# Kernel tuning notes

Measured on AMD Instinct MI355X. Metric: run time of the kernel, lower is better.

Reference implementation:

```python
import jax, jax.numpy as jnp
import numpy as np

C_IN = 512
C_QK = C_IN // 8
B, H, W = 8, 96, 96


def setup_inputs() -> dict:
    key = jax.random.key(0)
    ks = jax.random.split(key, 8)
    s = 1.0 / np.sqrt(C_IN)
    return {
        "x": jax.random.normal(ks[0], (B, C_IN, H, W), dtype=jnp.float32),
        "Wq": jax.random.normal(ks[1], (C_QK, C_IN), dtype=jnp.float32) * s,
        "bq": jnp.zeros((C_QK,), dtype=jnp.float32),
        "Wk": jax.random.normal(ks[2], (C_QK, C_IN), dtype=jnp.float32) * s,
        "bk": jnp.zeros((C_QK,), dtype=jnp.float32),
        "Wv": jax.random.normal(ks[3], (C_IN, C_IN), dtype=jnp.float32) * s,
        "bv": jnp.zeros((C_IN,), dtype=jnp.float32),
        "gamma": jnp.zeros((1,), dtype=jnp.float32),
    }


def reference(x, Wq, bq, Wk, bk, Wv, bv, gamma):
    Bb, Cc, Hh, Ww = x.shape
    # 1x1 convs as channel GEMMs
    q = jnp.einsum('bchw,oc->bohw', x, Wq) + bq[None, :, None, None]
    k = jnp.einsum('bchw,oc->bohw', x, Wk) + bk[None, :, None, None]
    v = jnp.einsum('bchw,oc->bohw', x, Wv) + bv[None, :, None, None]
    # vertical (column) energy: query at (h,w) vs keys at (g,w); diag h==g masked to -inf
    eH = jnp.einsum('bchw,bcgw->bhwg', q, k)  # [B,H,W,H]
    diag = jnp.eye(Hh, dtype=bool)[:, None, :]  # [H,1,H] broadcasts over w
    eH = jnp.where(diag[None], -jnp.inf, eH)
    # horizontal (row) energy: query at (h,w) vs keys at (h,u)
    eW = jnp.einsum('bchw,bchu->bhwu', q, k)  # [B,H,W,W]
    # joint softmax over concatenated H+W axis
    att = jax.nn.softmax(jnp.concatenate([eH, eW], axis=-1), axis=-1)
    aH, aW = att[..., :Hh], att[..., Hh:]
    out_H = jnp.einsum('bhwg,bcgw->bchw', aH, v)
    out_W = jnp.einsum('bhwu,bchu->bchw', aW, v)
    return gamma * (out_H + out_W) + x
```

## Files before the change

### kernel.cpp

```cpp
#include <hip/hip_runtime.h>
#include <math.h>

constexpr int nB = 8;
constexpr int nC = 512;
constexpr int nH = 96;
constexpr int nW = 96;
constexpr int nP = nH * nW;
constexpr int nCQK = 64;
constexpr int nS = nH + nW;
constexpr int nO = 640;
constexpr int nM = nB * nP;

using short8  = __attribute__((ext_vector_type(8))) short;
using ushort8 = __attribute__((ext_vector_type(8))) unsigned short;
using floatx4 = __attribute__((ext_vector_type(4))) float;

__device__ inline unsigned pack_bf16(float a, float b) {
    unsigned ua = __float_as_uint(a), ub = __float_as_uint(b);
    ua = (ua + 0x7fff + ((ua >> 16) & 1)) >> 16;
    ub = (ub + 0x7fff + ((ub >> 16) & 1)) >> 16;
    return ua | (ub << 16);
}
__device__ inline ushort f2bf(float a) {
    unsigned ua = __float_as_uint(a);
    return (ushort)((ua + 0x7fff + ((ua >> 16) & 1)) >> 16);
}
__device__ inline float bf2f(ushort u) {
    return __uint_as_float((unsigned)u << 16);
}

typedef __attribute__((address_space(3))) unsigned int lds_u32;
typedef __attribute__((address_space(1))) const unsigned int glb_u32;
__device__ inline void gl_lds16(const void* g, void* l) {
    __builtin_amdgcn_global_load_lds((glb_u32*)g, (lds_u32*)l, 16, 0, 0);
}

__global__ __launch_bounds__(256) void transpose_kernel(
    const float* __restrict__ x, ushort* __restrict__ xT)
{
    __shared__ float T[64 * 65];
    const int b = blockIdx.z, p0 = blockIdx.x * 64, c0 = blockIdx.y * 64;
    const int tid = threadIdx.x;
    #pragma unroll
    for (int it = 0; it < 4; ++it) {
        int c  = it * 16 + (tid >> 4);
        int p4 = (tid & 15) * 4;
        float4 v = *(const float4*)&x[((size_t)b * nC + c0 + c) * nP + p0 + p4];
        T[c * 65 + p4 + 0] = v.x; T[c * 65 + p4 + 1] = v.y;
        T[c * 65 + p4 + 2] = v.z; T[c * 65 + p4 + 3] = v.w;
    }
    __syncthreads();
    #pragma unroll
    for (int it = 0; it < 8; ++it) {
        int idx = it * 256 + tid;
        int p = idx >> 5;
        int c = (idx & 31) * 2;
        unsigned u = pack_bf16(T[c * 65 + p], T[(c + 1) * 65 + p]);
        *(unsigned*)&xT[((size_t)b * nP + p0 + p) * nC + c0 + c] = u;
    }
}

__global__ __launch_bounds__(256) void wconv_kernel(
    const float* __restrict__ Wq, const float* __restrict__ bq,
    const float* __restrict__ Wk, const float* __restrict__ bk,
    const float* __restrict__ Wv, const float* __restrict__ bv,
    ushort* __restrict__ Wc, float* __restrict__ bc)
{
    const int o = blockIdx.x, t = threadIdx.x;
    const float *src, *bsrc; int oo;
    if (o < 64)       { src = Wq; bsrc = bq; oo = o; }
    else if (o < 128) { src = Wk; bsrc = bk; oo = o - 64; }
    else              { src = Wv; bsrc = bv; oo = o - 128; }
    float2 v = *(const float2*)&src[(size_t)oo * nC + t * 2];
    *(unsigned*)&Wc[(size_t)o * nC + t * 2] = pack_bf16(v.x, v.y);
    if (t == 0) bc[o] = bsrc[oo];
}

__global__ __launch_bounds__(256) void mfma_proj_kernel(
    const ushort* __restrict__ xT, const ushort* __restrict__ Wc,
    const float* __restrict__ bc, float* __restrict__ qk,
    ushort* __restrict__ vW)
{
    __shared__ ushort As[3][128 * 32];
    __shared__ ushort Bs[3][128 * 32];
    const int tid = threadIdx.x;

    constexpr int NWG   = (nM / 128) * (nO / 128);
    constexpr int CHUNK = NWG / 8;
    const int bid = blockIdx.x;
    const int wg  = (bid & 7) * CHUNK + (bid >> 3);
    const int mtile = wg / 5, ntile = wg % 5;
    const int m0 = mtile * 128, o0 = ntile * 128;

    const int lane = tid & 63;
    const int wave = tid >> 6;

    const int srow = wave * 16 + (lane >> 2);
    const int schk = ((lane & 3) ^ ((lane >> 3) & 3)) * 8;
    const ushort* gA0 = xT + (size_t)(m0 + srow) * nC + schk;
    const ushort* gA1 = gA0 + (size_t)64 * nC;
    const ushort* gB0 = Wc + (size_t)(o0 + srow) * nC + schk;
    const ushort* gB1 = gB0 + (size_t)64 * nC;
    const int lbase  = wave * 16 * 32;
    const int lbase1 = lbase + 64 * 32;

    const int wr = wave & 1, wcl = wave >> 1;
    const int lm = lane & 15, q = lane >> 4;
    const int rsw = (lm >> 1) & 3;
    int aoff[4], boff[4];
    #pragma unroll
    for (int i = 0; i < 4; ++i)
        aoff[i] = (wr * 64 + i * 16 + lm) * 32 + ((q ^ rsw) * 8);
    #pragma unroll
    for (int j = 0; j < 4; ++j)
        boff[j] = (wcl * 64 + j * 16 + lm) * 32 + ((q ^ rsw) * 8);

    floatx4 acc[4][4];
    #pragma unroll
    for (int i = 0; i < 4; ++i)
        #pragma unroll
        for (int j = 0; j < 4; ++j) acc[i][j] = (floatx4){0.f, 0.f, 0.f, 0.f};

    const bool vmode = (ntile != 0);

    gl_lds16(gA0, &As[0][lbase]); gl_lds16(gA1, &As[0][lbase1]);
    gl_lds16(gB0, &Bs[0][lbase]); gl_lds16(gB1, &Bs[0][lbase1]);
    gl_lds16(gA0 + 32, &As[1][lbase]); gl_lds16(gA1 + 32, &As[1][lbase1]);
    gl_lds16(gB0 + 32, &Bs[1][lbase]); gl_lds16(gB1 + 32, &Bs[1][lbase1]);

    #pragma unroll
    for (int t = 0; t < 16; ++t) {
        if (t < 15) asm volatile("s_waitcnt vmcnt(4)" ::: "memory");
        else        asm volatile("s_waitcnt vmcnt(0)" ::: "memory");
        __builtin_amdgcn_s_barrier();
        __builtin_amdgcn_sched_barrier(0);
        if (t < 14) {
            const int nb = (t + 2) % 3;
            const int k0 = (t + 2) * 32;
            gl_lds16(gA0 + k0, &As[nb][lbase]);
            gl_lds16(gA1 + k0, &As[nb][lbase1]);
            gl_lds16(gB0 + k0, &Bs[nb][lbase]);
            gl_lds16(gB1 + k0, &Bs[nb][lbase1]);
        }
        const int cur = t % 3;
        short8 av[4], bvv[4];
        #pragma unroll
        for (int i = 0; i < 4; ++i) av[i] = *(const short8*)&As[cur][aoff[i]];
        #pragma unroll
        for (int j = 0; j < 4; ++j) bvv[j] = *(const short8*)&Bs[cur][boff[j]];
        if (!vmode) {
            #pragma unroll
            for (int i = 0; i < 4; ++i)
                #pragma unroll
                for (int j = 0; j < 4; ++j)
                    acc[i][j] = __builtin_amdgcn_mfma_f32_16x16x32_bf16(
                        av[i], bvv[j], acc[i][j], 0, 0, 0);
        } else {
            #pragma unroll
            for (int i = 0; i < 4; ++i)
                #pragma unroll
                for (int j = 0; j < 4; ++j)
                    acc[i][j] = __builtin_amdgcn_mfma_f32_16x16x32_bf16(
                        bvv[i], av[j], acc[i][j], 0, 0, 0);
        }
    }

    if (!vmode) {
        float bj[4];
        #pragma unroll
        for (int j = 0; j < 4; ++j) bj[j] = bc[wcl * 64 + j * 16 + lm];
        #pragma unroll
        for (int i = 0; i < 4; ++i) {
            #pragma unroll
            for (int r = 0; r < 4; ++r) {
                int mrow = m0 + wr * 64 + i * 16 + q * 4 + r;
                float* orow = qk + (size_t)mrow * 128 + wcl * 64 + lm;
                #pragma unroll
                for (int j = 0; j < 4; ++j) orow[j * 16] = acc[i][j][r] + bj[j];
            }
        }
    } else {
        const int b  = m0 / nP;
        const int p0 = m0 - b * nP;
        #pragma unroll
        for (int i = 0; i < 4; ++i) {
            #pragma unroll
            for (int r = 0; r < 4; ++r) {
                int o = o0 + wcl * 64 + i * 16 + q * 4 + r;
                float bias = bc[o];
                int c = o - 128;
                ushort* vrow = vW + ((size_t)(b * nC + c)) * nP + p0 + wr * 64 + lm;
                #pragma unroll
                for (int j = 0; j < 4; ++j)
                    vrow[j * 16] = f2bf(acc[i][j][r] + bias);
            }
        }
    }
}

__global__ __launch_bounds__(256) void vtrans_kernel(
    const ushort* __restrict__ vW, ushort* __restrict__ vH)
{
    __shared__ ushort T[96 * 128];
    const int c = blockIdx.x, b = blockIdx.y, tid = threadIdx.x;
    const size_t base = ((size_t)(b * nC + c)) * nP;
    for (int l = tid; l < 96 * 12; l += 256) {
        int hh = l / 12, seg = l % 12;
        uint4 u = *(const uint4*)&vW[base + (size_t)hh * nW + seg * 8];
        *(uint4*)&T[hh * 128 + ((seg ^ ((hh >> 3) & 7)) * 8)] = u;
    }
    __syncthreads();
    for (int l = tid; l < 96 * 12; l += 256) {
        int ww = l / 12, seg = l % 12;
        ushort8 vv;
        #pragma unroll
        for (int e = 0; e < 8; ++e) {
            int hh = seg * 8 + e;
            int phys = (((ww >> 3) ^ ((hh >> 3) & 7)) * 8) + (ww & 7);
            vv[e] = T[hh * 128 + phys];
        }
        *(ushort8*)&vH[base + (size_t)ww * nH + seg * 8] = vv;
    }
}

__global__ __launch_bounds__(256) void score_kernel(
    const float* __restrict__ qk, float* __restrict__ att, int mode)
{
    __shared__ float Qs[96][68];
    __shared__ float Ks[96][68];
    const int b   = blockIdx.y;
    const int fix = blockIdx.x;
    const int tid = threadIdx.x;

    for (int l = tid; l < 96 * 16; l += 256) {
        int r  = l / 16;
        int c4 = (l % 16) * 4;
        size_t p = (mode == 0) ? ((size_t)r * nW + fix) : ((size_t)fix * nW + r);
        const float* row = &qk[((size_t)b * nP + p) * 128];
        *(float4*)&Qs[r][c4] = *(const float4*)&row[c4];
        *(float4*)&Ks[r][c4] = *(const float4*)&row[64 + c4];
    }
    __syncthreads();

    const int tx = tid % 16;
    const int ty = tid / 16;
    float acc[6][6] = {};
    for (int c4 = 0; c4 < nCQK; c4 += 4) {
        float4 qv[6], kv[6];
        #pragma unroll
        for (int i = 0; i < 6; ++i) qv[i] = *(const float4*)&Qs[ty + 16 * i][c4];
        #pragma unroll
        for (int j = 0; j < 6; ++j) kv[j] = *(const float4*)&Ks[tx + 16 * j][c4];
        #pragma unroll
        for (int i = 0; i < 6; ++i)
            #pragma unroll
            for (int j = 0; j < 6; ++j)
                acc[i][j] += qv[i].x * kv[j].x + qv[i].y * kv[j].y
                           + qv[i].z * kv[j].z + qv[i].w * kv[j].w;
    }

    #pragma unroll
    for (int i = 0; i < 6; ++i) {
        int row = ty + 16 * i;
        #pragma unroll
        for (int j = 0; j < 6; ++j) {
            int col = tx + 16 * j;
            float val = acc[i][j];
            if (mode == 0) {
                if (col == row) val = -INFINITY;
                att[((size_t)b * nP + row * nW + fix) * nS + col] = val;
            } else {
                att[((size_t)b * nP + fix * nW + row) * nS + 96 + col] = val;
            }
        }
    }
}

__global__ __launch_bounds__(256) void softmax_kernel(
    const float* __restrict__ att, ushort* __restrict__ attb)
{
    const int wav  = threadIdx.x / 64;
    const int lane = threadIdx.x % 64;
    const size_t pix = (size_t)blockIdx.x * 4 + wav;
    const float* a = att + pix * nS;
    ushort* ab = attb + pix * nS;
    float v0 = a[lane], v1 = a[lane + 64], v2 = a[lane + 128];
    float m = fmaxf(fmaxf(v0, v1), v2);
    #pragma unroll
    for (int off = 32; off; off >>= 1) m = fmaxf(m, __shfl_xor(m, off));
    float e0 = __expf(v0 - m), e1 = __expf(v1 - m), e2 = __expf(v2 - m);
    float s = e0 + e1 + e2;
    #pragma unroll
    for (int off = 32; off; off >>= 1) s += __shfl_xor(s, off);
    float inv = 1.0f / s;
    ab[lane]       = f2bf(e0 * inv);
    ab[lane + 64]  = f2bf(e1 * inv);
    ab[lane + 128] = f2bf(e2 * inv);
}

__global__ __launch_bounds__(256) void aggH_kernel(
    const ushort* __restrict__ attb, const ushort* __restrict__ vH,
    ushort* __restrict__ oh)
{
    __shared__ ushort As[96 * 104];
    __shared__ ushort Bs[128 * 104];
    const int b = blockIdx.y, w = blockIdx.x, tid = threadIdx.x;

    for (int l = tid; l < 96 * 12; l += 256) {
        int h = l / 12, seg = l % 12;
        uint4 u = *(const uint4*)&attb[((size_t)(b * nP + h * nW + w)) * nS + seg * 8];
        *(uint4*)&As[h * 104 + seg * 8] = u;
    }
    const int lane = tid & 63, wave = tid >> 6;
    const int wr = wave & 1, wc = wave >> 1;
    const int lm = lane & 15, q = lane >> 4;
    int aoff[3], boff[4];
    #pragma unroll
    for (int i = 0; i < 3; ++i) aoff[i] = (wr * 48 + i * 16 + lm) * 104 + q * 8;
    #pragma unroll
    for (int j = 0; j < 4; ++j) boff[j] = (wc * 64 + j * 16 + lm) * 104 + q * 8;

    for (int ct = 0; ct < 4; ++ct) {
        if (ct) __syncthreads();
        for (int l = tid; l < 128 * 12; l += 256) {
            int cl = l / 12, seg = l % 12;
            uint4 u = *(const uint4*)&vH[((size_t)(b * nC + ct * 128 + cl)) * nP
                                         + w * nH + seg * 8];
            *(uint4*)&Bs[cl * 104 + seg * 8] = u;
        }
        __syncthreads();
        floatx4 acc[3][4];
        #pragma unroll
        for (int i = 0; i < 3; ++i)
            #pragma unroll
            for (int j = 0; j < 4; ++j) acc[i][j] = (floatx4){0.f, 0.f, 0.f, 0.f};
        #pragma unroll
        for (int ks = 0; ks < 3; ++ks) {
            short8 av[3], bvv[4];
            #pragma unroll
            for (int i = 0; i < 3; ++i) av[i] = *(const short8*)&As[aoff[i] + ks * 32];
            #pragma unroll
            for (int j = 0; j < 4; ++j) bvv[j] = *(const short8*)&Bs[boff[j] + ks * 32];
            #pragma unroll
            for (int i = 0; i < 3; ++i)
                #pragma unroll
                for (int j = 0; j < 4; ++j)
                    acc[i][j] = __builtin_amdgcn_mfma_f32_16x16x32_bf16(
                        av[i], bvv[j], acc[i][j], 0, 0, 0);
        }
        #pragma unroll
        for (int i = 0; i < 3; ++i) {
            #pragma unroll
            for (int r = 0; r < 4; ++r) {
                int h = wr * 48 + i * 16 + q * 4 + r;
                ushort* orow = oh + ((size_t)(b * nP + h * nW + w)) * nC
                               + ct * 128 + wc * 64 + lm;
                #pragma unroll
                for (int j = 0; j < 4; ++j) orow[j * 16] = f2bf(acc[i][j][r]);
            }
        }
    }
}

__global__ __launch_bounds__(256) void aggW_kernel(
    const ushort* __restrict__ attb, const ushort* __restrict__ vW,
    const ushort* __restrict__ oh, const float* __restrict__ x,
    const float* __restrict__ gamma, float* __restrict__ out)
{
    __shared__ ushort As[96 * 104];
    __shared__ ushort Bs[64 * 104];
    __shared__ ushort Os[96 * 72];
    const int b = blockIdx.y, h = blockIdx.x, tid = threadIdx.x;
    const float gm = gamma[0];

    for (int l = tid; l < 96 * 12; l += 256) {
        int ww = l / 12, seg = l % 12;
        uint4 u = *(const uint4*)&attb[((size_t)(b * nP + h * nW + ww)) * nS
                                       + 96 + seg * 8];
        *(uint4*)&As[ww * 104 + seg * 8] = u;
    }
    const int lane = tid & 63, wave = tid >> 6;
    const int wr = wave & 1, wc = wave >> 1;
    const int lm = lane & 15, q = lane >> 4;
    int coff[2], woff[3];
    #pragma unroll
    for (int i = 0; i < 2; ++i) coff[i] = (wc * 32 + i * 16 + lm) * 104 + q * 8;
    #pragma unroll
    for (int j = 0; j < 3; ++j) woff[j] = (wr * 48 + j * 16 + lm) * 104 + q * 8;

    for (int ct = 0; ct < 8; ++ct) {
        if (ct) __syncthreads();
        for (int l = tid; l < 64 * 12; l += 256) {
            int cl = l / 12, seg = l % 12;
            uint4 u = *(const uint4*)&vW[((size_t)(b * nC + ct * 64 + cl)) * nP
                                         + h * nW + seg * 8];
            *(uint4*)&Bs[cl * 104 + seg * 8] = u;
        }
        for (int l = tid; l < 96 * 8; l += 256) {
            int ww = l / 8, seg = l % 8;
            uint4 u = *(const uint4*)&oh[((size_t)(b * nP + h * nW + ww)) * nC
                                         + ct * 64 + seg * 8];
            *(uint4*)&Os[ww * 72 + seg * 8] = u;
        }
        __syncthreads();
        floatx4 acc[2][3];
        #pragma unroll
        for (int i = 0; i < 2; ++i)
            #pragma unroll
            for (int j = 0; j < 3; ++j) acc[i][j] = (floatx4){0.f, 0.f, 0.f, 0.f};
        #pragma unroll
        for (int ks = 0; ks < 3; ++ks) {
            short8 cv[2], wv[3];
            #pragma unroll
            for (int i = 0; i < 2; ++i) cv[i] = *(const short8*)&Bs[coff[i] + ks * 32];
            #pragma unroll
            for (int j = 0; j < 3; ++j) wv[j] = *(const short8*)&As[woff[j] + ks * 32];
            #pragma unroll
            for (int i = 0; i < 2; ++i)
                #pragma unroll
                for (int j = 0; j < 3; ++j)
                    acc[i][j] = __builtin_amdgcn_mfma_f32_16x16x32_bf16(
                        cv[i], wv[j], acc[i][j], 0, 0, 0);
        }
        #pragma unroll
        for (int i = 0; i < 2; ++i) {
            #pragma unroll
            for (int r = 0; r < 4; ++r) {
                int cl = wc * 32 + i * 16 + q * 4 + r;
                int c  = ct * 64 + cl;
                #pragma unroll
                for (int j = 0; j < 3; ++j) {
                    int ww = wr * 48 + j * 16 + lm;
                    size_t oidx = ((size_t)(b * nC + c) * nH + h) * nW + ww;
                    float ohv = bf2f(Os[ww * 72 + cl]);
                    out[oidx] = gm * (acc[i][j][r] + ohv) + x[oidx];
                }
            }
        }
    }
}

extern "C" void kernel_launch(void* const* d_in, const int* in_sizes, int n_in,
                              void* d_out, int out_size, void* d_ws, size_t ws_size,
                              hipStream_t stream)
{
    const float* x     = (const float*)d_in[0];
    const float* Wq    = (const float*)d_in[1];
    const float* bq    = (const float*)d_in[2];
    const float* Wk    = (const float*)d_in[3];
    const float* bk    = (const float*)d_in[4];
    const float* Wv    = (const float*)d_in[5];
    const float* bv    = (const float*)d_in[6];
    const float* gamma = (const float*)d_in[7];
    float* out = (float*)d_out;

    char* p = (char*)d_ws;
    ushort* xT  = (ushort*)p;
    ushort* vH  = (ushort*)p;
    p += (size_t)nM * nC * 2;
    float* qk   = (float*)p;
    p += (size_t)nM * 128 * 4;
    ushort* vW  = (ushort*)p;
    p += (size_t)nM * nC * 2;
    float* att  = (float*)p;
    ushort* Wc  = (ushort*)p;
    float* bc   = (float*)(p + (size_t)nO * nC * 2);
    p += (size_t)nM * nS * 4;
    ushort* attb = (ushort*)p;
    p += (size_t)nM * nS * 2;
    ushort* oh  = (ushort*)p;

    dim3 blk(256);
    transpose_kernel<<<dim3(nP / 64, nC / 64, nB), blk, 0, stream>>>(x, xT);
    wconv_kernel<<<dim3(nO), blk, 0, stream>>>(Wq, bq, Wk, bk, Wv, bv, Wc, bc);
    mfma_proj_kernel<<<dim3((nM / 128) * (nO / 128)), blk, 0, stream>>>(xT, Wc, bc, qk, vW);
    vtrans_kernel<<<dim3(nC, nB), blk, 0, stream>>>(vW, vH);
    score_kernel<<<dim3(nW, nB), blk, 0, stream>>>(qk, att, 0);
    score_kernel<<<dim3(nH, nB), blk, 0, stream>>>(qk, att, 1);
    softmax_kernel<<<dim3(nB * nP / 4), blk, 0, stream>>>(att, attb);
    aggH_kernel<<<dim3(nW, nB), blk, 0, stream>>>(attb, vH, oh);
    aggW_kernel<<<dim3(nH, nB), blk, 0, stream>>>(attb, vW, oh, x, gamma, out);
}
```

Baseline: 573.7 us.

## Vectorize stores via LDS staging and deepen projection GEMM pipeline to four buffers

The transpose kernel now writes 16-byte bf16 vectors instead of 4-byte pairs. The projection GEMM moves from a 3-stage to a 4-stage LDS prefetch ring with adjusted vmcnt waits. aggH and aggW stage their MFMA outputs through LDS so global stores (and the x reads in aggW) become coalesced 16-byte accesses instead of scattered 2- or 4-byte writes. This costs extra barriers and LDS reuse; aggW's float staging aliases its Bs/Os buffers.

```diff
diff --git a/kernel.cpp b/kernel.cpp
--- a/kernel.cpp
+++ b/kernel.cpp
@@ -51,12 +51,14 @@
     }
     __syncthreads();
     #pragma unroll
-    for (int it = 0; it < 8; ++it) {
+    for (int it = 0; it < 2; ++it) {
         int idx = it * 256 + tid;
-        int p = idx >> 5;
-        int c = (idx & 31) * 2;
-        unsigned u = pack_bf16(T[c * 65 + p], T[(c + 1) * 65 + p]);
-        *(unsigned*)&xT[((size_t)b * nP + p0 + p) * nC + c0 + c] = u;
+        int p  = idx >> 3;
+        int cc = (idx & 7) * 8;
+        ushort8 v;
+        #pragma unroll
+        for (int e = 0; e < 8; ++e) v[e] = f2bf(T[(cc + e) * 65 + p]);
+        *(ushort8*)&xT[((size_t)b * nP + p0 + p) * nC + c0 + cc] = v;
     }
 }
 
@@ -81,8 +83,8 @@
     const float* __restrict__ bc, float* __restrict__ qk,
     ushort* __restrict__ vW)
 {
-    __shared__ ushort As[3][128 * 32];
-    __shared__ ushort Bs[3][128 * 32];
+    __shared__ ushort As[4][128 * 32];
+    __shared__ ushort Bs[4][128 * 32];
     const int tid = threadIdx.x;
 
     constexpr int NWG   = (nM / 128) * (nO / 128);
@@ -123,26 +125,30 @@
 
     const bool vmode = (ntile != 0);
 
-    gl_lds16(gA0, &As[0][lbase]); gl_lds16(gA1, &As[0][lbase1]);
-    gl_lds16(gB0, &Bs[0][lbase]); gl_lds16(gB1, &Bs[0][lbase1]);
-    gl_lds16(gA0 + 32, &As[1][lbase]); gl_lds16(gA1 + 32, &As[1][lbase1]);
-    gl_lds16(gB0 + 32, &Bs[1][lbase]); gl_lds16(gB1 + 32, &Bs[1][lbase1]);
+    #pragma unroll
+    for (int tt = 0; tt < 3; ++tt) {
+        gl_lds16(gA0 + tt * 32, &As[tt][lbase]);
+        gl_lds16(gA1 + tt * 32, &As[tt][lbase1]);
+        gl_lds16(gB0 + tt * 32, &Bs[tt][lbase]);
+        gl_lds16(gB1 + tt * 32, &Bs[tt][lbase1]);
+    }
 
     #pragma unroll
     for (int t = 0; t < 16; ++t) {
-        if (t < 15) asm volatile("s_waitcnt vmcnt(4)" ::: "memory");
-        else        asm volatile("s_waitcnt vmcnt(0)" ::: "memory");
+        if (t <= 13)      asm volatile("s_waitcnt vmcnt(8)" ::: "memory");
+        else if (t == 14) asm volatile("s_waitcnt vmcnt(4)" ::: "memory");
+        else              asm volatile("s_waitcnt vmcnt(0)" ::: "memory");
         __builtin_amdgcn_s_barrier();
         __builtin_amdgcn_sched_barrier(0);
-        if (t < 14) {
-            const int nb = (t + 2) % 3;
-            const int k0 = (t + 2) * 32;
+        if (t < 13) {
+            const int nb = (t + 3) & 3;
+            const int k0 = (t + 3) * 32;
             gl_lds16(gA0 + k0, &As[nb][lbase]);
             gl_lds16(gA1 + k0, &As[nb][lbase1]);
             gl_lds16(gB0 + k0, &Bs[nb][lbase]);
             gl_lds16(gB1 + k0, &Bs[nb][lbase1]);
         }
-        const int cur = t % 3;
+        const int cur = t & 3;
         short8 av[4], bvv[4];
         #pragma unroll
         for (int i = 0; i < 4; ++i) av[i] = *(const short8*)&As[cur][aoff[i]];
@@ -304,6 +310,7 @@
 {
     __shared__ ushort As[96 * 104];
     __shared__ ushort Bs[128 * 104];
+    ushort* Ot = Bs;
     const int b = blockIdx.y, w = blockIdx.x, tid = threadIdx.x;
 
     for (int l = tid; l < 96 * 12; l += 256) {
@@ -348,16 +355,22 @@
                     acc[i][j] = __builtin_amdgcn_mfma_f32_16x16x32_bf16(
                         av[i], bvv[j], acc[i][j], 0, 0, 0);
         }
+        __syncthreads();
         #pragma unroll
         for (int i = 0; i < 3; ++i) {
             #pragma unroll
             for (int r = 0; r < 4; ++r) {
                 int h = wr * 48 + i * 16 + q * 4 + r;
-                ushort* orow = oh + ((size_t)(b * nP + h * nW + w)) * nC
-                               + ct * 128 + wc * 64 + lm;
-                #pragma unroll
-                for (int j = 0; j < 4; ++j) orow[j * 16] = f2bf(acc[i][j][r]);
+                #pragma unroll
+                for (int j = 0; j < 4; ++j)
+                    Ot[h * 136 + wc * 64 + j * 16 + lm] = f2bf(acc[i][j][r]);
             }
+        }
+        __syncthreads();
+        for (int l = tid; l < 96 * 16; l += 256) {
+            int h = l >> 4, seg = l & 15;
+            *(ushort8*)&oh[((size_t)(b * nP + h * nW + w)) * nC + ct * 128 + seg * 8] =
+                *(const ushort8*)&Ot[h * 136 + seg * 8];
         }
     }
 }
@@ -368,8 +381,10 @@
     const float* __restrict__ gamma, float* __restrict__ out)
 {
     __shared__ ushort As[96 * 104];
-    __shared__ ushort Bs[64 * 104];
-    __shared__ ushort Os[96 * 72];
+    __shared__ ushort BO[64 * 104 + 96 * 72];
+    ushort* Bs = BO;
+    ushort* Os = BO + 64 * 104;
+    float*  Ot = (float*)BO;
     const int b = blockIdx.y, h = blockIdx.x, tid = threadIdx.x;
     const float gm = gamma[0];
 
@@ -422,20 +437,37 @@
                     acc[i][j] = __builtin_amdgcn_mfma_f32_16x16x32_bf16(
                         cv[i], wv[j], acc[i][j], 0, 0, 0);
         }
-        #pragma unroll
-        for (int i = 0; i < 2; ++i) {
+        float sv[2][3][4];
+        #pragma unroll
+        for (int i = 0; i < 2; ++i)
             #pragma unroll
             for (int r = 0; r < 4; ++r) {
                 int cl = wc * 32 + i * 16 + q * 4 + r;
-                int c  = ct * 64 + cl;
                 #pragma unroll
                 for (int j = 0; j < 3; ++j) {
                     int ww = wr * 48 + j * 16 + lm;
-                    size_t oidx = ((size_t)(b * nC + c) * nH + h) * nW + ww;
-                    float ohv = bf2f(Os[ww * 72 + cl]);
-                    out[oidx] = gm * (acc[i][j][r] + ohv) + x[oidx];
+                    sv[i][j][r] = gm * (acc[i][j][r] + bf2f(Os[ww * 72 + cl]));
                 }
             }
+        __syncthreads();
+        #pragma unroll
+        for (int i = 0; i < 2; ++i)
+            #pragma unroll
+            for (int r = 0; r < 4; ++r) {
+                int cl = wc * 32 + i * 16 + q * 4 + r;
+                #pragma unroll
+                for (int j = 0; j < 3; ++j)
+                    Ot[cl * 100 + wr * 48 + j * 16 + lm] = sv[i][j][r];
+            }
+        __syncthreads();
+        for (int l = tid; l < 64 * 24; l += 256) {
+            int cl = l / 24, w4 = (l % 24) * 4;
+            size_t gidx = ((size_t)(b * nC + ct * 64 + cl) * nH + h) * nW + w4;
+            float4 xv = *(const float4*)&x[gidx];
+            float4 s4 = *(const float4*)&Ot[cl * 100 + w4];
+            float4 ov = make_float4(s4.x + xv.x, s4.y + xv.y,
+                                    s4.z + xv.z, s4.w + xv.w);
+            *(float4*)&out[gidx] = ov;
         }
     }
 }
```

Result: no change. 567.1 us (-1.1%).
